# Kernel tuning notes

Hardware: AMD Instinct MI355X
Metric: run time of the kernel (lower is better)

The kernel has to match this reference:

```python
import jax, jax.numpy as jnp
import numpy as np

W_PULL = 1.0
W_PUSH = 1.0
W_NORM = 0.001
W_EDGE = 10.0
DELTA_V = 0.5
DELTA_D = 1.5
CE_W = 1.0
DICE_W = 1.0
IGN = -100
NUM_CLASSES = 8
EMBED_DIM = 16
NUM_INST = 16  # instance ids 1..16, 0 = background
EPS_C = 1e-8
EPS_D = 1e-5


def setup_inputs() -> dict:
    key = jax.random.key(0)
    k1, k2, k3, k4 = jax.random.split(key, 4)
    B, D, H, W = 2, 64, 128, 128
    return {
        "sem_logits": jax.random.normal(k1, (B, NUM_CLASSES, D, H, W), jnp.float32),
        "instance_embed": jax.random.normal(k2, (B, EMBED_DIM, D, H, W), jnp.float32),
        "class_labels": jax.random.randint(k3, (B, D, H, W), 0, NUM_CLASSES, dtype=jnp.int32),
        "labels": jax.random.randint(k4, (B, D, H, W), 0, NUM_INST + 1, dtype=jnp.int32),
    }


def _ce_loss(logits, target):
    # nn.CrossEntropyLoss(ignore_index=-100), mean over valid voxels
    logp = jax.nn.log_softmax(logits, axis=1)
    valid = (target != IGN)
    t_safe = jnp.where(valid, target, 0)
    nll = -jnp.take_along_axis(logp, t_safe[:, None].astype(jnp.int32), axis=1)[:, 0]
    v = valid.astype(logits.dtype)
    return (nll * v).sum() / jnp.maximum(v.sum(), 1.0)


def _dice_loss(logits, target):
    C = logits.shape[1]
    probs = jax.nn.softmax(logits, axis=1)
    valid = (target != IGN)
    t_safe = jnp.where(valid, target, 0)
    one_hot = jax.nn.one_hot(t_safe, C, dtype=probs.dtype, axis=1)  # [B,C,D,H,W]
    vm = valid[:, None].astype(probs.dtype)
    probs = probs * vm
    one_hot = one_hot * vm
    axes = tuple(range(2, probs.ndim))
    inter = (probs * one_hot).sum(axes)
    card_p = probs.sum(axes)
    card_g = one_hot.sum(axes)
    dice = (2.0 * inter + EPS_D) / (card_p + card_g + EPS_D)
    return 1.0 - dice.mean()


def _boundary_weight(labels):
    # morphological gradient: 3x3x3 max-pool minus min-pool, replicate pad
    lf = labels.astype(jnp.float32)
    p = jnp.pad(lf, ((0, 0), (1, 1), (1, 1), (1, 1)), mode='edge')
    mx = jax.lax.reduce_window(p, -jnp.inf, jax.lax.max, (1, 3, 3, 3), (1, 1, 1, 1), 'VALID')
    mn = jax.lax.reduce_window(p, jnp.inf, jax.lax.min, (1, 3, 3, 3), (1, 1, 1, 1), 'VALID')
    boundary = (mx != mn).astype(jnp.float32)
    return 1.0 + boundary * (W_EDGE - 1.0)


def _instance_loss(embed, labels, w):
    B, C = embed.shape[:2]
    e_flat = embed.reshape(B, C, -1)   # [B,C,N]
    l_flat = labels.reshape(B, -1)     # [B,N]
    w_flat = w.reshape(B, -1)          # [B,N] (w_bone == 1 since weight_bone==1.0)
    K = NUM_INST

    def per_batch(e, l, wv):
        seg = lambda x: jax.ops.segment_sum(x, l, num_segments=K + 1)
        wsum = seg(wv)                       # [K+1]
        cnt = seg(jnp.ones_like(wv))         # [K+1]
        cnum = seg((e * wv).T)               # [K+1, C]
        centers = cnum / (wsum[:, None] + EPS_C)
        cg = centers[l]                      # [N, C] gather own-instance center
        dist = jnp.linalg.norm(e.T - cg, axis=-1)
        pull_sum = seg(jax.nn.relu(dist - DELTA_V) ** 2 * wv)
        present = cnt[1:] > 0                # ids 1..K
        loss_pull = jnp.where(present, pull_sum[1:] / jnp.maximum(cnt[1:], 1.0), 0.0).sum()
        c = centers[1:]                      # [K, C]
        iu, ju = jnp.triu_indices(K, k=1)
        pw = jnp.linalg.norm(c[iu] - c[ju], axis=-1)
        pv = (present[iu] & present[ju]).astype(pw.dtype)
        npres = present.sum().astype(pw.dtype)
        npairs = npres * (npres - 1.0) / 2.0
        push = jax.nn.relu(2.0 * DELTA_D - pw) ** 2 * pv
        loss_push = jnp.where(npairs > 0, push.sum() / jnp.maximum(npairs, 1.0), 0.0)
        cn = jnp.linalg.norm(c, axis=-1)
        loss_norm = jnp.where(npres > 0, (cn * present).sum() / jnp.maximum(npres, 1.0), 0.0)
        return loss_pull, loss_push, loss_norm, (npres > 0).astype(jnp.float32)

    lp, lpu, ln, val = jax.vmap(per_batch)(e_flat, l_flat, w_flat)
    n = jnp.maximum(val.sum(), 1.0)
    return (W_PULL * lp.sum() + W_PUSH * lpu.sum() + W_NORM * ln.sum()) / n


def reference(sem_logits, instance_embed, class_labels, labels):
    loss_ce = _ce_loss(sem_logits, class_labels)
    loss_dice = _dice_loss(sem_logits, class_labels)
    loss_sem = CE_W * loss_ce + DICE_W * loss_dice
    w_edge = _boundary_weight(labels)
    # weight_bone == 1.0 -> w_bone = ones (scipy EDT branch disabled by module guard)
    loss_ins = _instance_loss(instance_embed, labels, w_edge)
    loss = loss_sem + loss_ins
    return loss, loss_sem, loss_ce, loss_dice, loss_ins
```

## Files before the change

### kernel.cpp

```cpp
#include <hip/hip_runtime.h>

#define DHW (64*128*128)
#define MIR 32

#define OFF_CEM   0
#define OFF_SEGM  1568
#define OFF_PULLM 21152
#define OFF_CTR   22240
#define OFF_CNT   22784
#define ACC_FLOATS 22818

typedef __bf16 bf16x8 __attribute__((ext_vector_type(8)));
typedef float f32x4 __attribute__((ext_vector_type(4)));
union FragU { short s[8]; bf16x8 v; };

__device__ inline short f2bf(float f) {
    union { float f; unsigned u; } v; v.f = f;
    unsigned r = v.u + 0x7FFF + ((v.u >> 16) & 1);
    return (short)(r >> 16);
}

__device__ inline unsigned edge4(const int* __restrict__ L, int vb, int4 c) {
    int x = vb & 127, y = (vb >> 7) & 127, z = vb >> 14;
    int z0 = max(z - 1, 0), z1 = min(z + 1, 63);
    int y0 = max(y - 1, 0), y1 = min(y + 1, 127);
    int xm = max(x - 1, 0), xp = min(x + 4, 127);
    unsigned b0 = 0, b1 = 0, b2 = 0, b3 = 0;
    for (int zz = z0; zz <= z1; ++zz) {
        for (int yy = y0; yy <= y1; ++yy) {
            const int* row = L + (zz << 14) + (yy << 7);
            int4 r = *reinterpret_cast<const int4*>(&row[x]);
            int rm = row[xm], rp = row[xp];
            b0 |= (rm != c.x) | (r.x != c.x) | (r.y != c.x);
            b1 |= (r.x != c.y) | (r.y != c.y) | (r.z != c.y);
            b2 |= (r.y != c.z) | (r.z != c.z) | (r.w != c.z);
            b3 |= (r.z != c.w) | (r.w != c.w) | (rp != c.w);
            if (b0 & b1 & b2 & b3) return 0xF;
        }
    }
    return b0 | (b1 << 1) | (b2 << 2) | (b3 << 3);
}

__global__ void zero_kernel(float* acc) {
    int i = blockIdx.x * 1024 + threadIdx.x;
    if (i < ACC_FLOATS) acc[i] = 0.0f;
}

__global__ __launch_bounds__(256) void front_kernel(const float* __restrict__ logits,
                                                    const float* __restrict__ embed,
                                                    const int* __restrict__ cls,
                                                    const int* __restrict__ labels,
                                                    float* __restrict__ acc) {
    __shared__ float sh[25];
    __shared__ float cacc[288];
    int role = blockIdx.x & 1;
    int pos = blockIdx.x >> 1;
    int b = pos & 1;
    int blk = pos >> 1;
    int mir = blk & (MIR - 1);
    int tid = threadIdx.x;

    if (role == 0) {
        int vb = (blk * 256 + tid) * 4;
        const float* lg = logits + (size_t)b * 8 * DHW;
        const int* cl = cls + (size_t)b * DHW;

        float4 xc[8];
#pragma unroll
        for (int c = 0; c < 8; ++c)
            xc[c] = *reinterpret_cast<const float4*>(&lg[(size_t)c * DHW + vb]);
        int4 t4 = *reinterpret_cast<const int4*>(&cl[vb]);
        int tt[4] = {t4.x, t4.y, t4.z, t4.w};

        float nll = 0.f, cardp[8], inter[8], cardg[8];
#pragma unroll
        for (int c = 0; c < 8; ++c) { cardp[c] = 0.f; inter[c] = 0.f; cardg[c] = 0.f; }

#pragma unroll
        for (int j = 0; j < 4; ++j) {
            float x[8];
#pragma unroll
            for (int c = 0; c < 8; ++c) x[c] = ((const float*)&xc[c])[j];
            int t = tt[j];
            bool valid = (t != -100);
            float mx = x[0];
#pragma unroll
            for (int c = 1; c < 8; ++c) mx = fmaxf(mx, x[c]);
            float e[8], s = 0.f;
#pragma unroll
            for (int c = 0; c < 8; ++c) { e[c] = __expf(x[c] - mx); s += e[c]; }
            float inv = 1.0f / s;
            float lse = __logf(s);
            if (valid) {
#pragma unroll
                for (int c = 0; c < 8; ++c) {
                    float p = e[c] * inv;
                    cardp[c] += p;
                    if (t == c) { inter[c] += p; cardg[c] += 1.f; nll += mx + lse - x[c]; }
                }
            }
        }

        if (tid < 25) sh[tid] = 0.f;
        __syncthreads();
        int lane = tid & 63;
        float vals[25];
        vals[0] = nll;
#pragma unroll
        for (int c = 0; c < 8; ++c) { vals[1 + c] = cardp[c]; vals[9 + c] = inter[c]; vals[17 + c] = cardg[c]; }
#pragma unroll
        for (int i = 0; i < 25; ++i) {
            float r = vals[i];
#pragma unroll
            for (int off = 32; off > 0; off >>= 1) r += __shfl_down(r, off, 64);
            if (lane == 0) atomicAdd(&sh[i], r);
        }
        __syncthreads();
        if (tid < 25) {
            int dst;
            if (tid == 0) dst = 0;
            else if (tid < 9) dst = 1 + b * 8 + (tid - 1);
            else if (tid < 17) dst = 17 + b * 8 + (tid - 9);
            else dst = 33 + b * 8 + (tid - 17);
            atomicAdd(&acc[OFF_CEM + mir * 49 + dst], sh[tid]);
        }
    } else {
        int lane = tid & 63;
        int wv = tid >> 6;
        int m = lane & 15;
        int quad = lane >> 4;

        const int* L = labels + (size_t)b * DHW;
        const float* E = embed + (size_t)b * 16 * DHW + (size_t)m * DHW;

        int waveId = blk * 4 + wv;
        int off = waveId * 256 + quad * 8;

        f32x4 acc_c = {0.f, 0.f, 0.f, 0.f};
        f32x4 acc_w = {0.f, 0.f, 0.f, 0.f};
        f32x4 acc_n = {0.f, 0.f, 0.f, 0.f};

        FragU ones_col;
#pragma unroll
        for (int j = 0; j < 8; ++j) ones_col.s[j] = (m == 0) ? (short)0x3F80 : (short)0;

        int4 l0 = *reinterpret_cast<const int4*>(&L[off]);
        int4 l1 = *reinterpret_cast<const int4*>(&L[off + 4]);
        float4 f0 = *reinterpret_cast<const float4*>(&E[off]);
        float4 f1 = *reinterpret_cast<const float4*>(&E[off + 4]);

        for (int i = 0; i < 8; ++i) {
            int4 nl0, nl1; float4 nf0, nf1;
            if (i < 7) {
                int noff = off + 32;
                nl0 = *reinterpret_cast<const int4*>(&L[noff]);
                nl1 = *reinterpret_cast<const int4*>(&L[noff + 4]);
                nf0 = *reinterpret_cast<const float4*>(&E[noff]);
                nf1 = *reinterpret_cast<const float4*>(&E[noff + 4]);
            }
            unsigned eb = edge4(L, off, l0) | (edge4(L, off + 4, l1) << 4);

            int ls[8] = {l0.x, l0.y, l0.z, l0.w, l1.x, l1.y, l1.z, l1.w};
            float fs[8] = {f0.x, f0.y, f0.z, f0.w, f1.x, f1.y, f1.z, f1.w};

            FragU a, a2, bf;
#pragma unroll
            for (int j = 0; j < 8; ++j) {
                short w = ((eb >> j) & 1) ? (short)0x4120 : (short)0x3F80;
                bool hit = (ls[j] == m + 1);
                a.s[j]  = hit ? w : (short)0;
                a2.s[j] = hit ? (short)0x3F80 : (short)0;
                bf.s[j] = f2bf(fs[j]);
            }
            acc_c = __builtin_amdgcn_mfma_f32_16x16x32_bf16(a.v, bf.v, acc_c, 0, 0, 0);
            acc_w = __builtin_amdgcn_mfma_f32_16x16x32_bf16(a.v, ones_col.v, acc_w, 0, 0, 0);
            acc_n = __builtin_amdgcn_mfma_f32_16x16x32_bf16(a2.v, ones_col.v, acc_n, 0, 0, 0);

            l0 = nl0; l1 = nl1; f0 = nf0; f1 = nf1;
            off += 32;
        }

        for (int i = tid; i < 288; i += 256) cacc[i] = 0.f;
        __syncthreads();
#pragma unroll
        for (int r = 0; r < 4; ++r)
            atomicAdd(&cacc[(quad * 4 + r) * 16 + m], acc_c[r]);
        if (m == 0) {
#pragma unroll
            for (int r = 0; r < 4; ++r) {
                atomicAdd(&cacc[256 + quad * 4 + r], acc_w[r]);
                atomicAdd(&cacc[272 + quad * 4 + r], acc_n[r]);
            }
        }
        __syncthreads();
        {
            float* segbase = acc + OFF_SEGM + mir * 612 + b * 306;
            atomicAdd(&segbase[16 + tid], cacc[tid]);
            if (tid < 16) atomicAdd(&segbase[272 + 1 + tid], cacc[256 + tid]);
            else if (tid < 32) atomicAdd(&segbase[289 + 1 + (tid - 16)], cacc[256 + tid]);
        }
    }
}

__global__ __launch_bounds__(1024) void centers_kernel(float* acc) {
    int tid = threadIdx.x;
    if (tid < 544) {
        int b = tid / 272, r = tid % 272;
        int k = r >> 4;
        float cn = 0.f, ws = 0.f;
        for (int mv = 0; mv < MIR; ++mv) {
            const float* segbase = acc + OFF_SEGM + mv * 612 + b * 306;
            if (r >= 16) cn += segbase[r];
            ws += segbase[272 + k];
        }
        acc[OFF_CTR + tid] = (r >= 16) ? cn / (ws + 1e-8f) : 0.f;
    } else if (tid < 578) {
        int j = tid - 544;
        int b = j / 17, k = j % 17;
        float s = 0.f;
        for (int mv = 0; mv < MIR; ++mv)
            s += acc[OFF_SEGM + mv * 612 + b * 306 + 289 + k];
        acc[OFF_CNT + j] = s;
    }
}

__global__ __launch_bounds__(256) void pull_kernel(const float* __restrict__ embed,
                                                   const int* __restrict__ labels,
                                                   float* __restrict__ acc) {
    int b = blockIdx.x & 1;
    int blk = blockIdx.x >> 1;
    int tid = threadIdx.x;
    int wv = tid >> 6;
    __shared__ float ctr[17 * 16];
    __shared__ float ps[4 * 20];
    for (int i = tid; i < 272; i += 256) ctr[i] = acc[OFF_CTR + b * 272 + i];
    for (int i = tid; i < 80; i += 256) ps[i] = 0.f;
    __syncthreads();

    const int* L = labels + (size_t)b * DHW;
    const float* E = embed + (size_t)b * 16 * DHW;
    int vb = (blk * 256 + tid) * 4;

    int4 l4 = *reinterpret_cast<const int4*>(&L[vb]);
    int l[4] = {l4.x, l4.y, l4.z, l4.w};

    float4 e4[16];
#pragma unroll
    for (int c = 0; c < 16; ++c)
        e4[c] = *reinterpret_cast<const float4*>(&E[(size_t)c * DHW + vb]);

    unsigned eb = edge4(L, vb, l4);

#pragma unroll
    for (int j = 0; j < 4; ++j) {
        if (l[j] != 0) {
            float w = ((eb >> j) & 1) ? 10.f : 1.f;
            const float4* cg = reinterpret_cast<const float4*>(&ctr[l[j] * 16]);
            float d2 = 0.f;
#pragma unroll
            for (int q = 0; q < 4; ++q) {
                float4 cv = cg[q];
                float d0 = ((const float*)&e4[4 * q + 0])[j] - cv.x;
                float d1 = ((const float*)&e4[4 * q + 1])[j] - cv.y;
                float dd2 = ((const float*)&e4[4 * q + 2])[j] - cv.z;
                float d3 = ((const float*)&e4[4 * q + 3])[j] - cv.w;
                d2 += d0 * d0 + d1 * d1 + dd2 * dd2 + d3 * d3;
            }
            float d = fmaxf(sqrtf(d2) - 0.5f, 0.f);
            atomicAdd(&ps[wv * 20 + l[j]], d * d * w);
        }
    }
    __syncthreads();
    if (tid >= 1 && tid < 17) {
        float v = ps[tid] + ps[20 + tid] + ps[40 + tid] + ps[60 + tid];
        int mir = blk & (MIR - 1);
        if (v != 0.f) atomicAdd(&acc[OFF_PULLM + mir * 34 + b * 17 + tid], v);
    }
}

__global__ __launch_bounds__(256) void finalize_kernel(const float* __restrict__ acc, float* __restrict__ out) {
    __shared__ float s_ce[49], s_pl[34];
    __shared__ float sh_push[2], sh_norm[2], sh_pull[2], sh_npres[2];
    int tid = threadIdx.x;
    if (tid < 49) {
        float s = 0.f;
        for (int mv = 0; mv < MIR; ++mv) s += acc[OFF_CEM + mv * 49 + tid];
        s_ce[tid] = s;
    }
    if (tid >= 64 && tid < 98) {
        int j = tid - 64;
        float s = 0.f;
        for (int mv = 0; mv < MIR; ++mv) s += acc[OFF_PULLM + mv * 34 + j];
        s_pl[j] = s;
    }
    if (tid < 2) { sh_push[tid] = 0.f; sh_norm[tid] = 0.f; sh_pull[tid] = 0.f; sh_npres[tid] = 0.f; }
    __syncthreads();

    if (tid < 32) {
        int b = tid >> 4, k = (tid & 15) + 1;
        float cnt = acc[OFF_CNT + b * 17 + k];
        if (cnt > 0.f) {
            atomicAdd(&sh_npres[b], 1.f);
            atomicAdd(&sh_pull[b], s_pl[b * 17 + k] / fmaxf(cnt, 1.f));
            const float* c = &acc[OFF_CTR + (b * 17 + k) * 16];
            float n2 = 0.f;
            for (int i = 0; i < 16; ++i) n2 += c[i] * c[i];
            atomicAdd(&sh_norm[b], sqrtf(n2));
        }
    }
    for (int t = tid; t < 240; t += blockDim.x) {
        int b = t / 120, p = t % 120;
        int i = 1, rem = p;
        while (rem >= (16 - i)) { rem -= (16 - i); ++i; }
        int j = i + 1 + rem;
        bool pi = acc[OFF_CNT + b * 17 + i] > 0.f;
        bool pj = acc[OFF_CNT + b * 17 + j] > 0.f;
        if (pi && pj) {
            const float* ci = &acc[OFF_CTR + (b * 17 + i) * 16];
            const float* cj = &acc[OFF_CTR + (b * 17 + j) * 16];
            float d2 = 0.f;
            for (int c = 0; c < 16; ++c) { float dd = ci[c] - cj[c]; d2 += dd * dd; }
            float r = fmaxf(3.0f - sqrtf(d2), 0.f);
            atomicAdd(&sh_push[b], r * r);
        }
    }
    __syncthreads();
    if (tid == 0) {
        float nll = s_ce[0];
        float vcnt = 0.f;
        for (int i = 0; i < 16; ++i) vcnt += s_ce[33 + i];
        float ce = nll / fmaxf(vcnt, 1.f);
        float dsum = 0.f;
        for (int i = 0; i < 16; ++i) {
            float it = s_ce[17 + i], cp = s_ce[1 + i], cg = s_ce[33 + i];
            dsum += (2.f * it + 1e-5f) / (cp + cg + 1e-5f);
        }
        float dice = 1.f - dsum / 16.f;
        float lp = 0.f, lpu = 0.f, ln = 0.f, val = 0.f;
        for (int b = 0; b < 2; ++b) {
            float npres = sh_npres[b];
            lp += sh_pull[b];
            float npairs = npres * (npres - 1.f) * 0.5f;
            lpu += (npairs > 0.f) ? sh_push[b] / fmaxf(npairs, 1.f) : 0.f;
            ln += (npres > 0.f) ? sh_norm[b] / fmaxf(npres, 1.f) : 0.f;
            val += (npres > 0.f) ? 1.f : 0.f;
        }
        float n = fmaxf(val, 1.f);
        float ins = (1.0f * lp + 1.0f * lpu + 0.001f * ln) / n;
        float sem = ce + dice;
        out[0] = sem + ins;
        out[1] = sem;
        out[2] = ce;
        out[3] = dice;
        out[4] = ins;
    }
}

extern "C" void kernel_launch(void* const* d_in, const int* in_sizes, int n_in,
                              void* d_out, int out_size, void* d_ws, size_t ws_size,
                              hipStream_t stream) {
    const float* sem = (const float*)d_in[0];
    const float* emb = (const float*)d_in[1];
    const int* cls = (const int*)d_in[2];
    const int* lab = (const int*)d_in[3];
    float* out = (float*)d_out;
    float* acc = (float*)d_ws;

    hipLaunchKernelGGL(zero_kernel, dim3(23), dim3(1024), 0, stream, acc);
    hipLaunchKernelGGL(front_kernel, dim3(4096), dim3(256), 0, stream, sem, emb, cls, lab, acc);
    hipLaunchKernelGGL(centers_kernel, dim3(1), dim3(1024), 0, stream, acc);
    hipLaunchKernelGGL(pull_kernel, dim3(2048), dim3(256), 0, stream, emb, lab, acc);
    hipLaunchKernelGGL(finalize_kernel, dim3(1), dim3(256), 0, stream, acc, out);
}
```

Measured before the change: 354.1 us.

## Split CE work across both phases and share edge bits via wave shuffles

Cross-entropy/dice work is split in half: the first 512 block-groups per batch run alongside the segment-sum pass and the rest alongside the pull pass. This balances memory traffic between the two kernels that sit around the serial centers kernel. The segment pass now computes each voxel's boundary bits once per lane and distributes them with shuffles, instead of redoing the 3x3x3 neighbourhood check inside every MFMA iteration. The pull pass streams embedding channels in groups of four to cut register pressure. The block-index mapping with the divide-by-3 interleave adds complexity, and the per-wave edge-bit lane mapping must line up exactly.

```diff
diff --git a/kernel.cpp b/kernel.cpp
--- a/kernel.cpp
+++ b/kernel.cpp
@@ -46,159 +46,180 @@
     if (i < ACC_FLOATS) acc[i] = 0.0f;
 }
 
-__global__ __launch_bounds__(256) void front_kernel(const float* __restrict__ logits,
-                                                    const float* __restrict__ embed,
-                                                    const int* __restrict__ cls,
-                                                    const int* __restrict__ labels,
-                                                    float* __restrict__ acc) {
-    __shared__ float sh[25];
-    __shared__ float cacc[288];
-    int role = blockIdx.x & 1;
-    int pos = blockIdx.x >> 1;
-    int b = pos & 1;
-    int blk = pos >> 1;
+__device__ void ce_role(const float* __restrict__ logits, const int* __restrict__ cls,
+                        float* __restrict__ acc, int b, int blk, float* sh) {
+    int tid = threadIdx.x;
     int mir = blk & (MIR - 1);
+    int vb = (blk * 256 + tid) * 4;
+    const float* lg = logits + (size_t)b * 8 * DHW;
+    const int* cl = cls + (size_t)b * DHW;
+
+    float4 xc[8];
+#pragma unroll
+    for (int c = 0; c < 8; ++c)
+        xc[c] = *reinterpret_cast<const float4*>(&lg[(size_t)c * DHW + vb]);
+    int4 t4 = *reinterpret_cast<const int4*>(&cl[vb]);
+    int tt[4] = {t4.x, t4.y, t4.z, t4.w};
+
+    float nll = 0.f, cardp[8], inter[8], cardg[8];
+#pragma unroll
+    for (int c = 0; c < 8; ++c) { cardp[c] = 0.f; inter[c] = 0.f; cardg[c] = 0.f; }
+
+#pragma unroll
+    for (int j = 0; j < 4; ++j) {
+        float x[8];
+#pragma unroll
+        for (int c = 0; c < 8; ++c) x[c] = ((const float*)&xc[c])[j];
+        int t = tt[j];
+        bool valid = (t != -100);
+        float mx = x[0];
+#pragma unroll
+        for (int c = 1; c < 8; ++c) mx = fmaxf(mx, x[c]);
+        float e[8], s = 0.f;
+#pragma unroll
+        for (int c = 0; c < 8; ++c) { e[c] = __expf(x[c] - mx); s += e[c]; }
+        float inv = 1.0f / s;
+        float lse = __logf(s);
+        if (valid) {
+#pragma unroll
+            for (int c = 0; c < 8; ++c) {
+                float p = e[c] * inv;
+                cardp[c] += p;
+                if (t == c) { inter[c] += p; cardg[c] += 1.f; nll += mx + lse - x[c]; }
+            }
+        }
+    }
+
+    if (tid < 25) sh[tid] = 0.f;
+    __syncthreads();
+    int lane = tid & 63;
+    float vals[25];
+    vals[0] = nll;
+#pragma unroll
+    for (int c = 0; c < 8; ++c) { vals[1 + c] = cardp[c]; vals[9 + c] = inter[c]; vals[17 + c] = cardg[c]; }
+#pragma unroll
+    for (int i = 0; i < 25; ++i) {
+        float r = vals[i];
+#pragma unroll
+        for (int off = 32; off > 0; off >>= 1) r += __shfl_down(r, off, 64);
+        if (lane == 0) atomicAdd(&sh[i], r);
+    }
+    __syncthreads();
+    if (tid < 25) {
+        int dst;
+        if (tid == 0) dst = 0;
+        else if (tid < 9) dst = 1 + b * 8 + (tid - 1);
+        else if (tid < 17) dst = 17 + b * 8 + (tid - 9);
+        else dst = 33 + b * 8 + (tid - 17);
+        atomicAdd(&acc[OFF_CEM + mir * 49 + dst], sh[tid]);
+    }
+}
+
+__global__ __launch_bounds__(256) void phaseA_kernel(const float* __restrict__ logits,
+                                                     const float* __restrict__ embed,
+                                                     const int* __restrict__ cls,
+                                                     const int* __restrict__ labels,
+                                                     float* __restrict__ acc) {
+    __shared__ float smem[352];
+    int x = blockIdx.x;
+    int g = x / 3, r3 = x % 3;
     int tid = threadIdx.x;
 
-    if (role == 0) {
-        int vb = (blk * 256 + tid) * 4;
-        const float* lg = logits + (size_t)b * 8 * DHW;
-        const int* cl = cls + (size_t)b * DHW;
-
-        float4 xc[8];
-#pragma unroll
-        for (int c = 0; c < 8; ++c)
-            xc[c] = *reinterpret_cast<const float4*>(&lg[(size_t)c * DHW + vb]);
-        int4 t4 = *reinterpret_cast<const int4*>(&cl[vb]);
-        int tt[4] = {t4.x, t4.y, t4.z, t4.w};
-
-        float nll = 0.f, cardp[8], inter[8], cardg[8];
-#pragma unroll
-        for (int c = 0; c < 8; ++c) { cardp[c] = 0.f; inter[c] = 0.f; cardg[c] = 0.f; }
-
-#pragma unroll
-        for (int j = 0; j < 4; ++j) {
-            float x[8];
-#pragma unroll
-            for (int c = 0; c < 8; ++c) x[c] = ((const float*)&xc[c])[j];
-            int t = tt[j];
-            bool valid = (t != -100);
-            float mx = x[0];
-#pragma unroll
-            for (int c = 1; c < 8; ++c) mx = fmaxf(mx, x[c]);
-            float e[8], s = 0.f;
-#pragma unroll
-            for (int c = 0; c < 8; ++c) { e[c] = __expf(x[c] - mx); s += e[c]; }
-            float inv = 1.0f / s;
-            float lse = __logf(s);
-            if (valid) {
-#pragma unroll
-                for (int c = 0; c < 8; ++c) {
-                    float p = e[c] * inv;
-                    cardp[c] += p;
-                    if (t == c) { inter[c] += p; cardg[c] += 1.f; nll += mx + lse - x[c]; }
-                }
-            }
-        }
-
-        if (tid < 25) sh[tid] = 0.f;
-        __syncthreads();
-        int lane = tid & 63;
-        float vals[25];
-        vals[0] = nll;
-#pragma unroll
-        for (int c = 0; c < 8; ++c) { vals[1 + c] = cardp[c]; vals[9 + c] = inter[c]; vals[17 + c] = cardg[c]; }
-#pragma unroll
-        for (int i = 0; i < 25; ++i) {
-            float r = vals[i];
-#pragma unroll
-            for (int off = 32; off > 0; off >>= 1) r += __shfl_down(r, off, 64);
-            if (lane == 0) atomicAdd(&sh[i], r);
-        }
-        __syncthreads();
-        if (tid < 25) {
-            int dst;
-            if (tid == 0) dst = 0;
-            else if (tid < 9) dst = 1 + b * 8 + (tid - 1);
-            else if (tid < 17) dst = 17 + b * 8 + (tid - 9);
-            else dst = 33 + b * 8 + (tid - 17);
-            atomicAdd(&acc[OFF_CEM + mir * 49 + dst], sh[tid]);
-        }
-    } else {
-        int lane = tid & 63;
-        int wv = tid >> 6;
-        int m = lane & 15;
-        int quad = lane >> 4;
-
-        const int* L = labels + (size_t)b * DHW;
-        const float* E = embed + (size_t)b * 16 * DHW + (size_t)m * DHW;
-
-        int waveId = blk * 4 + wv;
-        int off = waveId * 256 + quad * 8;
-
-        f32x4 acc_c = {0.f, 0.f, 0.f, 0.f};
-        f32x4 acc_w = {0.f, 0.f, 0.f, 0.f};
-        f32x4 acc_n = {0.f, 0.f, 0.f, 0.f};
-
-        FragU ones_col;
-#pragma unroll
-        for (int j = 0; j < 8; ++j) ones_col.s[j] = (m == 0) ? (short)0x3F80 : (short)0;
-
-        int4 l0 = *reinterpret_cast<const int4*>(&L[off]);
-        int4 l1 = *reinterpret_cast<const int4*>(&L[off + 4]);
-        float4 f0 = *reinterpret_cast<const float4*>(&E[off]);
-        float4 f1 = *reinterpret_cast<const float4*>(&E[off + 4]);
-
-        for (int i = 0; i < 8; ++i) {
-            int4 nl0, nl1; float4 nf0, nf1;
-            if (i < 7) {
-                int noff = off + 32;
-                nl0 = *reinterpret_cast<const int4*>(&L[noff]);
-                nl1 = *reinterpret_cast<const int4*>(&L[noff + 4]);
-                nf0 = *reinterpret_cast<const float4*>(&E[noff]);
-                nf1 = *reinterpret_cast<const float4*>(&E[noff + 4]);
-            }
-            unsigned eb = edge4(L, off, l0) | (edge4(L, off + 4, l1) << 4);
-
-            int ls[8] = {l0.x, l0.y, l0.z, l0.w, l1.x, l1.y, l1.z, l1.w};
-            float fs[8] = {f0.x, f0.y, f0.z, f0.w, f1.x, f1.y, f1.z, f1.w};
-
-            FragU a, a2, bf;
-#pragma unroll
-            for (int j = 0; j < 8; ++j) {
-                short w = ((eb >> j) & 1) ? (short)0x4120 : (short)0x3F80;
-                bool hit = (ls[j] == m + 1);
-                a.s[j]  = hit ? w : (short)0;
-                a2.s[j] = hit ? (short)0x3F80 : (short)0;
-                bf.s[j] = f2bf(fs[j]);
-            }
-            acc_c = __builtin_amdgcn_mfma_f32_16x16x32_bf16(a.v, bf.v, acc_c, 0, 0, 0);
-            acc_w = __builtin_amdgcn_mfma_f32_16x16x32_bf16(a.v, ones_col.v, acc_w, 0, 0, 0);
-            acc_n = __builtin_amdgcn_mfma_f32_16x16x32_bf16(a2.v, ones_col.v, acc_n, 0, 0, 0);
-
-            l0 = nl0; l1 = nl1; f0 = nf0; f1 = nf1;
-            off += 32;
-        }
-
-        for (int i = tid; i < 288; i += 256) cacc[i] = 0.f;
-        __syncthreads();
-#pragma unroll
-        for (int r = 0; r < 4; ++r)
-            atomicAdd(&cacc[(quad * 4 + r) * 16 + m], acc_c[r]);
-        if (m == 0) {
-#pragma unroll
-            for (int r = 0; r < 4; ++r) {
-                atomicAdd(&cacc[256 + quad * 4 + r], acc_w[r]);
-                atomicAdd(&cacc[272 + quad * 4 + r], acc_n[r]);
-            }
-        }
-        __syncthreads();
-        {
-            float* segbase = acc + OFF_SEGM + mir * 612 + b * 306;
-            atomicAdd(&segbase[16 + tid], cacc[tid]);
-            if (tid < 16) atomicAdd(&segbase[272 + 1 + tid], cacc[256 + tid]);
-            else if (tid < 32) atomicAdd(&segbase[289 + 1 + (tid - 16)], cacc[256 + tid]);
-        }
+    if (r3 == 2) {
+        int ce_idx = g;
+        ce_role(logits, cls, acc, ce_idx >> 9, (ce_idx & 511), smem);
+        return;
+    }
+    int seg_idx = g * 2 + r3;
+    int b = seg_idx & 1;
+    int blk = seg_idx >> 1;
+    int mir = blk & (MIR - 1);
+    int lane = tid & 63;
+    int wv = tid >> 6;
+    int m = lane & 15;
+    int quad = lane >> 4;
+
+    const int* L = labels + (size_t)b * DHW;
+    const float* E = embed + (size_t)b * 16 * DHW + (size_t)m * DHW;
+
+    int waveId = blk * 4 + wv;
+    int wavebase = waveId * 256;
+
+    unsigned eb_own;
+    {
+        int own_off = wavebase + lane * 4;
+        int4 lo = *reinterpret_cast<const int4*>(&L[own_off]);
+        eb_own = edge4(L, own_off, lo);
+    }
+
+    int off = wavebase + quad * 8;
+
+    f32x4 acc_c = {0.f, 0.f, 0.f, 0.f};
+    f32x4 acc_w = {0.f, 0.f, 0.f, 0.f};
+    f32x4 acc_n = {0.f, 0.f, 0.f, 0.f};
+
+    FragU ones_col;
+#pragma unroll
+    for (int j = 0; j < 8; ++j) ones_col.s[j] = (m == 0) ? (short)0x3F80 : (short)0;
+
+    int4 l0 = *reinterpret_cast<const int4*>(&L[off]);
+    int4 l1 = *reinterpret_cast<const int4*>(&L[off + 4]);
+    float4 f0 = *reinterpret_cast<const float4*>(&E[off]);
+    float4 f1 = *reinterpret_cast<const float4*>(&E[off + 4]);
+
+    for (int i = 0; i < 8; ++i) {
+        int4 nl0, nl1; float4 nf0, nf1;
+        if (i < 7) {
+            int noff = off + 32;
+            nl0 = *reinterpret_cast<const int4*>(&L[noff]);
+            nl1 = *reinterpret_cast<const int4*>(&L[noff + 4]);
+            nf0 = *reinterpret_cast<const float4*>(&E[noff]);
+            nf1 = *reinterpret_cast<const float4*>(&E[noff + 4]);
+        }
+        int s0 = i * 8 + quad * 2;
+        unsigned ebA = (unsigned)__shfl((int)eb_own, s0, 64);
+        unsigned ebB = (unsigned)__shfl((int)eb_own, s0 + 1, 64);
+        unsigned eb = (ebA & 0xF) | ((ebB & 0xF) << 4);
+
+        int ls[8] = {l0.x, l0.y, l0.z, l0.w, l1.x, l1.y, l1.z, l1.w};
+        float fs[8] = {f0.x, f0.y, f0.z, f0.w, f1.x, f1.y, f1.z, f1.w};
+
+        FragU a, a2, bf;
+#pragma unroll
+        for (int j = 0; j < 8; ++j) {
+            short w = ((eb >> j) & 1) ? (short)0x4120 : (short)0x3F80;
+            bool hit = (ls[j] == m + 1);
+            a.s[j]  = hit ? w : (short)0;
+            a2.s[j] = hit ? (short)0x3F80 : (short)0;
+            bf.s[j] = f2bf(fs[j]);
+        }
+        acc_c = __builtin_amdgcn_mfma_f32_16x16x32_bf16(a.v, bf.v, acc_c, 0, 0, 0);
+        acc_w = __builtin_amdgcn_mfma_f32_16x16x32_bf16(a.v, ones_col.v, acc_w, 0, 0, 0);
+        acc_n = __builtin_amdgcn_mfma_f32_16x16x32_bf16(a2.v, ones_col.v, acc_n, 0, 0, 0);
+
+        l0 = nl0; l1 = nl1; f0 = nf0; f1 = nf1;
+        off += 32;
+    }
+
+    float* cacc = smem;
+    for (int i = tid; i < 288; i += 256) cacc[i] = 0.f;
+    __syncthreads();
+#pragma unroll
+    for (int r = 0; r < 4; ++r)
+        atomicAdd(&cacc[(quad * 4 + r) * 16 + m], acc_c[r]);
+    if (m == 0) {
+#pragma unroll
+        for (int r = 0; r < 4; ++r) {
+            atomicAdd(&cacc[256 + quad * 4 + r], acc_w[r]);
+            atomicAdd(&cacc[272 + quad * 4 + r], acc_n[r]);
+        }
+    }
+    __syncthreads();
+    {
+        float* segbase = acc + OFF_SEGM + mir * 612 + b * 306;
+        atomicAdd(&segbase[16 + tid], cacc[tid]);
+        if (tid < 16) atomicAdd(&segbase[272 + 1 + tid], cacc[256 + tid]);
+        else if (tid < 32) atomicAdd(&segbase[289 + 1 + (tid - 16)], cacc[256 + tid]);
     }
 }
 
@@ -224,15 +245,27 @@
     }
 }
 
-__global__ __launch_bounds__(256) void pull_kernel(const float* __restrict__ embed,
-                                                   const int* __restrict__ labels,
-                                                   float* __restrict__ acc) {
-    int b = blockIdx.x & 1;
-    int blk = blockIdx.x >> 1;
+__global__ __launch_bounds__(256) void phaseB_kernel(const float* __restrict__ logits,
+                                                     const float* __restrict__ embed,
+                                                     const int* __restrict__ cls,
+                                                     const int* __restrict__ labels,
+                                                     float* __restrict__ acc) {
+    __shared__ float smem[352];
+    int x = blockIdx.x;
+    int g = x / 3, r3 = x % 3;
     int tid = threadIdx.x;
+
+    if (r3 == 2) {
+        int ce_idx = g;
+        ce_role(logits, cls, acc, ce_idx >> 9, (ce_idx & 511) + 512, smem);
+        return;
+    }
+    int pull_idx = g * 2 + r3;
+    int b = pull_idx & 1;
+    int blk = pull_idx >> 1;
     int wv = tid >> 6;
-    __shared__ float ctr[17 * 16];
-    __shared__ float ps[4 * 20];
+    float* ctr = smem;
+    float* ps = smem + 272;
     for (int i = tid; i < 272; i += 256) ctr[i] = acc[OFF_CTR + b * 272 + i];
     for (int i = tid; i < 80; i += 256) ps[i] = 0.f;
     __syncthreads();
@@ -243,30 +276,33 @@
 
     int4 l4 = *reinterpret_cast<const int4*>(&L[vb]);
     int l[4] = {l4.x, l4.y, l4.z, l4.w};
-
-    float4 e4[16];
-#pragma unroll
-    for (int c = 0; c < 16; ++c)
-        e4[c] = *reinterpret_cast<const float4*>(&E[(size_t)c * DHW + vb]);
-
     unsigned eb = edge4(L, vb, l4);
+
+    float d2a[4] = {0.f, 0.f, 0.f, 0.f};
+#pragma unroll
+    for (int q = 0; q < 4; ++q) {
+        float4 e0 = *reinterpret_cast<const float4*>(&E[(size_t)(4 * q + 0) * DHW + vb]);
+        float4 e1 = *reinterpret_cast<const float4*>(&E[(size_t)(4 * q + 1) * DHW + vb]);
+        float4 e2 = *reinterpret_cast<const float4*>(&E[(size_t)(4 * q + 2) * DHW + vb]);
+        float4 e3 = *reinterpret_cast<const float4*>(&E[(size_t)(4 * q + 3) * DHW + vb]);
+#pragma unroll
+        for (int j = 0; j < 4; ++j) {
+            if (l[j] != 0) {
+                float4 cv = *reinterpret_cast<const float4*>(&ctr[l[j] * 16 + q * 4]);
+                float d0 = ((const float*)&e0)[j] - cv.x;
+                float d1 = ((const float*)&e1)[j] - cv.y;
+                float d2 = ((const float*)&e2)[j] - cv.z;
+                float d3 = ((const float*)&e3)[j] - cv.w;
+                d2a[j] += d0 * d0 + d1 * d1 + d2 * d2 + d3 * d3;
+            }
+        }
+    }
 
 #pragma unroll
     for (int j = 0; j < 4; ++j) {
         if (l[j] != 0) {
             float w = ((eb >> j) & 1) ? 10.f : 1.f;
-            const float4* cg = reinterpret_cast<const float4*>(&ctr[l[j] * 16]);
-            float d2 = 0.f;
-#pragma unroll
-            for (int q = 0; q < 4; ++q) {
-                float4 cv = cg[q];
-                float d0 = ((const float*)&e4[4 * q + 0])[j] - cv.x;
-                float d1 = ((const float*)&e4[4 * q + 1])[j] - cv.y;
-                float dd2 = ((const float*)&e4[4 * q + 2])[j] - cv.z;
-                float d3 = ((const float*)&e4[4 * q + 3])[j] - cv.w;
-                d2 += d0 * d0 + d1 * d1 + dd2 * dd2 + d3 * d3;
-            }
-            float d = fmaxf(sqrtf(d2) - 0.5f, 0.f);
+            float d = fmaxf(sqrtf(d2a[j]) - 0.5f, 0.f);
             atomicAdd(&ps[wv * 20 + l[j]], d * d * w);
         }
     }
@@ -367,8 +403,8 @@
     float* acc = (float*)d_ws;
 
     hipLaunchKernelGGL(zero_kernel, dim3(23), dim3(1024), 0, stream, acc);
-    hipLaunchKernelGGL(front_kernel, dim3(4096), dim3(256), 0, stream, sem, emb, cls, lab, acc);
+    hipLaunchKernelGGL(phaseA_kernel, dim3(3072), dim3(256), 0, stream, sem, emb, cls, lab, acc);
     hipLaunchKernelGGL(centers_kernel, dim3(1), dim3(1024), 0, stream, acc);
-    hipLaunchKernelGGL(pull_kernel, dim3(2048), dim3(256), 0, stream, emb, lab, acc);
+    hipLaunchKernelGGL(phaseB_kernel, dim3(3072), dim3(256), 0, stream, sem, emb, cls, lab, acc);
     hipLaunchKernelGGL(finalize_kernel, dim3(1), dim3(256), 0, stream, acc, out);
 }
```

After: 305.9 us. 1.16x faster.
